# Kernel optimization log

Hardware: AMD Instinct MI355X
Metric: run time of the kernel (lower is better)

Reference implementation:

```python
import jax, jax.numpy as jnp
import numpy as np

B, S, HID, NH, INTER, VOCAB = 8, 1024, 512, 8, 2048, 30522
EPS = 1e-12


def _layernorm(x, w, b):
    m = jnp.mean(x, axis=-1, keepdims=True)
    v = jnp.mean((x - m) ** 2, axis=-1, keepdims=True)
    return (x - m) * jax.lax.rsqrt(v + EPS) * w + b


def _multihead_mut(x, M):
    # x: (b, s, d); M: (H, s, s). Split d into H heads, mix along the
    # sequence axis per head: out[b,t,h,d] = sum_s x[b,s,h,d] * M[h,s,t]
    b, s, d = x.shape
    xh = x.reshape(b, s, NH, d // NH)
    out = jnp.einsum('bshd,hst->bthd', xh, M)
    return out.reshape(b, s, d)


def setup_inputs() -> dict:
    key = jax.random.key(0)
    ks = jax.random.split(key, 14)
    g = lambda i, shape, scale: jax.random.normal(ks[i], shape, dtype=jnp.float32) * scale
    return {
        'x': jax.random.randint(ks[0], (B, S), 0, VOCAB),
        'word_emb': g(1, (VOCAB, HID), 0.02),
        'pos_emb': g(2, (S, HID), 0.02),
        'tok_emb': g(3, (2, HID), 0.02),
        'emb_ln_w': jnp.ones((HID,), dtype=jnp.float32),
        'emb_ln_b': jnp.zeros((HID,), dtype=jnp.float32),
        'init_d': g(4, (INTER, HID), 0.02),
        'init_b': g(5, (INTER,), 0.02),
        'init_M': g(6, (NH, S, S), 1.0 / np.sqrt(S)),
        'inter0_d': g(7, (INTER, INTER), 1.0 / np.sqrt(INTER)),
        'inter0_b': g(8, (INTER,), 0.02),
        'inter0_M': g(9, (NH, S, S), 1.0 / np.sqrt(S)),
        'final_d': g(10, (HID, INTER), 1.0 / np.sqrt(INTER)),
        'final_b': g(11, (HID,), 0.02),
    }


def reference(x, word_emb, pos_emb, tok_emb, emb_ln_w, emb_ln_b,
              init_d, init_b, init_M, inter0_d, inter0_b, inter0_M,
              final_d, final_b):
    # BertEmbeddings: word + position + token_type(all zeros) -> LayerNorm
    emb = word_emb[x] + pos_emb[None, :, :] + tok_emb[0][None, None, :]
    xo = _layernorm(emb, emb_ln_w, emb_ln_b)  # (B, S, HID)

    # layer 0 (flattened): project to intermediate, per-head seq mix, bias, quad act
    xo = xo @ init_d.T                      # (B, S, INTER)
    xo = _multihead_mut(xo, init_M)
    xo = xo + init_b
    xo = xo * xo                            # activation_quad

    # layer 1 (flattened)
    xo = xo @ inter0_d.T                    # (B, S, INTER)
    xo = _multihead_mut(xo, inter0_M)
    xo = xo + inter0_b
    xo = xo * xo                            # activation_quad

    return xo @ final_d.T + final_b         # (B, S, HID)
```

## Files before the change

kernel.cpp:

```cpp
#include <hip/hip_runtime.h>

typedef _Float16 f16;
typedef _Float16 f16x4 __attribute__((ext_vector_type(4)));
typedef _Float16 f16x8 __attribute__((ext_vector_type(8)));
typedef float    f32x4 __attribute__((ext_vector_type(4)));

#define SEQ   1024
#define HID   512
#define NHEAD 8
#define DH    256
#define INTER 2048
#define BATCH 8
#define ROWS  (BATCH * SEQ)

__device__ __forceinline__ void mm_core(const f16* __restrict__ At,
                                        const f16* __restrict__ Bt,
                                        int K, f32x4 (&acc)[4][4]) {
  __shared__ __align__(16) f16 As[128 * 32];
  __shared__ __align__(16) f16 Bs[128 * 32];
  const int tid  = threadIdx.x;
  const int lane = tid & 63, wv = tid >> 6;
  const int wm = (wv >> 1) * 64, wn = (wv & 1) * 64;
  const int lrow  = lane & 15;
  const int kfrag = (lane >> 4) * 8;
  const int c1 = wv * 64 + lane;
  const int r1 = c1 >> 2, kq1 = (c1 & 3) * 8;
  const int r2 = r1 + 64;
  const int eoff = c1 * 8;
  const f16* Ap1 = At + (size_t)r1 * K + kq1;
  const f16* Ap2 = At + (size_t)r2 * K + kq1;
  const f16* Bp1 = Bt + (size_t)r1 * K + kq1;
  const f16* Bp2 = Bt + (size_t)r2 * K + kq1;
  int4 ra1 = *(const int4*)Ap1;
  int4 ra2 = *(const int4*)Ap2;
  int4 rb1 = *(const int4*)Bp1;
  int4 rb2 = *(const int4*)Bp2;
  for (int k0 = 0; k0 < K; k0 += 32) {
    __syncthreads();
    *(int4*)&As[eoff]        = ra1;
    *(int4*)&As[2048 + eoff] = ra2;
    *(int4*)&Bs[eoff]        = rb1;
    *(int4*)&Bs[2048 + eoff] = rb2;
    __syncthreads();
    if (k0 + 32 < K) {
      ra1 = *(const int4*)(Ap1 + k0 + 32);
      ra2 = *(const int4*)(Ap2 + k0 + 32);
      rb1 = *(const int4*)(Bp1 + k0 + 32);
      rb2 = *(const int4*)(Bp2 + k0 + 32);
    }
    f16x8 af[4], bf[4];
    #pragma unroll
    for (int t = 0; t < 4; ++t) {
      af[t] = *(const f16x8*)&As[(wm + t * 16 + lrow) * 32 + kfrag];
      bf[t] = *(const f16x8*)&Bs[(wn + t * 16 + lrow) * 32 + kfrag];
    }
    #pragma unroll
    for (int i = 0; i < 4; ++i)
      #pragma unroll
      for (int j = 0; j < 4; ++j)
        acc[i][j] = __builtin_amdgcn_mfma_f32_16x16x32_f16(af[i], bf[j],
                                                           acc[i][j], 0, 0, 0);
  }
}

__device__ __forceinline__ void zero_acc(f32x4 (&acc)[4][4]) {
  f32x4 z = {0.f, 0.f, 0.f, 0.f};
  #pragma unroll
  for (int i = 0; i < 4; ++i)
    #pragma unroll
    for (int j = 0; j < 4; ++j) acc[i][j] = z;
}

__global__ __launch_bounds__(256) void gemm_t_kernel(
    const f16* __restrict__ A, const f16* __restrict__ W,
    f16* __restrict__ Xt, int K) {
  int row0 = blockIdx.y * 128, col0 = blockIdx.x * 128;
  f32x4 acc[4][4];
  zero_acc(acc);
  mm_core(A + (size_t)row0 * K, W + (size_t)col0 * K, K, acc);
  int tid = threadIdx.x, lane = tid & 63, wv = tid >> 6;
  int wm = (wv >> 1) * 64, wn = (wv & 1) * 64;
  int cn = lane & 15, rbase = (lane >> 4) * 4;
  int b = row0 >> 10, sbase = row0 & 1023;
  #pragma unroll
  for (int mt = 0; mt < 4; ++mt) {
    int s = sbase + wm + mt * 16 + rbase;
    #pragma unroll
    for (int nt = 0; nt < 4; ++nt) {
      int n = col0 + wn + nt * 16 + cn;
      int h = n >> 8, d = n & 255;
      f16x4 v = {(f16)acc[mt][nt][0], (f16)acc[mt][nt][1],
                 (f16)acc[mt][nt][2], (f16)acc[mt][nt][3]};
      *(f16x4*)&Xt[(((size_t)(b * 8 + h) * 256 + d) << 10) + s] = v;
    }
  }
}

__global__ __launch_bounds__(256) void mut_kernel(
    const f16* __restrict__ Mt, const f16* __restrict__ Xt,
    const float* __restrict__ bias, f16* __restrict__ Y) {
  int b = blockIdx.z >> 3, h = blockIdx.z & 7;
  int t0 = blockIdx.y * 128, d0 = blockIdx.x * 128;
  f32x4 acc[4][4];
  zero_acc(acc);
  const f16* Ap = Mt + ((size_t)h << 20) + ((size_t)t0 << 10);
  const f16* Bp = Xt + (((size_t)(b * 8 + h) * 256 + d0) << 10);
  mm_core(Ap, Bp, SEQ, acc);
  int tid = threadIdx.x, lane = tid & 63, wv = tid >> 6;
  int wm = (wv >> 1) * 64, wn = (wv & 1) * 64;
  int cn = lane & 15, rbase = (lane >> 4) * 4;
  #pragma unroll
  for (int mt = 0; mt < 4; ++mt) {
    int t = t0 + wm + mt * 16 + rbase;
    #pragma unroll
    for (int nt = 0; nt < 4; ++nt) {
      int d = d0 + wn + nt * 16 + cn;
      float bb = bias[(h << 8) + d];
      size_t base = (((size_t)(b << 10) + t) << 11) + (h << 8) + d;
      #pragma unroll
      for (int r = 0; r < 4; ++r) {
        float v = acc[mt][nt][r] + bb;
        Y[base + (size_t)r * INTER] = (f16)(v * v);
      }
    }
  }
}

__global__ __launch_bounds__(256) void gemm_out_kernel(
    const f16* __restrict__ A, const f16* __restrict__ W,
    const float* __restrict__ bias, float* __restrict__ out, int K, int N) {
  int row0 = blockIdx.y * 128, col0 = blockIdx.x * 128;
  f32x4 acc[4][4];
  zero_acc(acc);
  mm_core(A + (size_t)row0 * K, W + (size_t)col0 * K, K, acc);
  int tid = threadIdx.x, lane = tid & 63, wv = tid >> 6;
  int wm = (wv >> 1) * 64, wn = (wv & 1) * 64;
  int cn = lane & 15, rbase = (lane >> 4) * 4;
  #pragma unroll
  for (int mt = 0; mt < 4; ++mt) {
    int r0 = row0 + wm + mt * 16 + rbase;
    #pragma unroll
    for (int nt = 0; nt < 4; ++nt) {
      int col = col0 + wn + nt * 16 + cn;
      float bb = bias[col];
      #pragma unroll
      for (int r = 0; r < 4; ++r)
        out[(size_t)(r0 + r) * N + col] = acc[mt][nt][r] + bb;
    }
  }
}

__global__ __launch_bounds__(256) void embed_ln_kernel(
    const int* __restrict__ x, const float* __restrict__ wemb,
    const float* __restrict__ pemb, const float* __restrict__ temb,
    const float* __restrict__ lnw, const float* __restrict__ lnb,
    f16* __restrict__ out) {
  int row = blockIdx.x;
  int s = row & (SEQ - 1);
  int tok = x[row];
  const float* we = wemb + (size_t)tok * HID;
  const float* pe = pemb + (size_t)s * HID;
  int c = threadIdx.x;
  float e0 = we[c] + pe[c] + temb[c];
  float e1 = we[c + 256] + pe[c + 256] + temb[c + 256];
  float s1 = e0 + e1, s2 = e0 * e0 + e1 * e1;
  #pragma unroll
  for (int off = 32; off > 0; off >>= 1) {
    s1 += __shfl_down(s1, off, 64);
    s2 += __shfl_down(s2, off, 64);
  }
  __shared__ float r1[4], r2[4];
  int wid = threadIdx.x >> 6, lane = threadIdx.x & 63;
  if (lane == 0) { r1[wid] = s1; r2[wid] = s2; }
  __syncthreads();
  float S1 = r1[0] + r1[1] + r1[2] + r1[3];
  float S2 = r2[0] + r2[1] + r2[2] + r2[3];
  float m = S1 * (1.0f / HID);
  float v = S2 * (1.0f / HID) - m * m;
  float inv = rsqrtf(v + 1e-12f);
  f16* o = out + (size_t)row * HID;
  o[c]       = (f16)((e0 - m) * inv * lnw[c]       + lnb[c]);
  o[c + 256] = (f16)((e1 - m) * inv * lnw[c + 256] + lnb[c + 256]);
}

__global__ __launch_bounds__(256) void cast_f16_kernel(
    const float* __restrict__ in, f16* __restrict__ out, int n) {
  int i = (blockIdx.x * 256 + threadIdx.x) * 4;
  if (i < n) {
    float4 v = *(const float4*)(in + i);
    f16x4 o = {(f16)v.x, (f16)v.y, (f16)v.z, (f16)v.w};
    *(f16x4*)(out + i) = o;
  }
}

__global__ __launch_bounds__(256) void mtrans_kernel(
    const float* __restrict__ M, f16* __restrict__ Mt) {
  __shared__ float T[32][33];
  int h = blockIdx.z;
  int s0 = blockIdx.y * 32, t0 = blockIdx.x * 32;
  int tx = threadIdx.x & 31, ty = threadIdx.x >> 5;
  const float* Mh = M + ((size_t)h << 20);
  #pragma unroll
  for (int i = 0; i < 32; i += 8)
    T[ty + i][tx] = Mh[((size_t)(s0 + ty + i) << 10) + t0 + tx];
  __syncthreads();
  f16* Mth = Mt + ((size_t)h << 20);
  #pragma unroll
  for (int i = 0; i < 32; i += 8)
    Mth[((size_t)(t0 + ty + i) << 10) + s0 + tx] = (f16)T[tx][ty + i];
}

extern "C" void kernel_launch(void* const* d_in, const int* in_sizes, int n_in,
                              void* d_out, int out_size, void* d_ws, size_t ws_size,
                              hipStream_t stream) {
  const int*   x        = (const int*)d_in[0];
  const float* wemb     = (const float*)d_in[1];
  const float* pemb     = (const float*)d_in[2];
  const float* temb     = (const float*)d_in[3];
  const float* lnw      = (const float*)d_in[4];
  const float* lnb      = (const float*)d_in[5];
  const float* init_d   = (const float*)d_in[6];
  const float* init_b   = (const float*)d_in[7];
  const float* init_M   = (const float*)d_in[8];
  const float* inter0_d = (const float*)d_in[9];
  const float* inter0_b = (const float*)d_in[10];
  const float* inter0_M = (const float*)d_in[11];
  const float* final_d  = (const float*)d_in[12];
  const float* final_b  = (const float*)d_in[13];
  float* out = (float*)d_out;

  char* ws = (char*)d_ws;
  f16* R0 = (f16*)(ws);
  f16* R1 = (f16*)(ws + 8388608);
  f16* R2 = (f16*)(ws + 10485760);
  f16* R3 = (f16*)(ws + 27262976);
  f16* R4 = (f16*)(ws + 60817408);
  f16* R5 = (f16*)(ws + 94371840);

  embed_ln_kernel<<<ROWS, 256, 0, stream>>>(x, wemb, pemb, temb, lnw, lnb, R0);
  cast_f16_kernel<<<(INTER * HID / 4 + 255) / 256, 256, 0, stream>>>(init_d, R1, INTER * HID);
  mtrans_kernel<<<dim3(32, 32, 8), 256, 0, stream>>>(init_M, R2);
  gemm_t_kernel<<<dim3(INTER / 128, ROWS / 128), 256, 0, stream>>>(R0, R1, R3, HID);
  mut_kernel<<<dim3(DH / 128, SEQ / 128, BATCH * NHEAD), 256, 0, stream>>>(R2, R3, init_b, R4);
  cast_f16_kernel<<<(INTER * INTER / 4 + 255) / 256, 256, 0, stream>>>(inter0_d, R0, INTER * INTER);
  mtrans_kernel<<<dim3(32, 32, 8), 256, 0, stream>>>(inter0_M, R2);
  gemm_t_kernel<<<dim3(INTER / 128, ROWS / 128), 256, 0, stream>>>(R4, R0, R5, INTER);
  mut_kernel<<<dim3(DH / 128, SEQ / 128, BATCH * NHEAD), 256, 0, stream>>>(R2, R5, inter0_b, R3);
  cast_f16_kernel<<<(HID * INTER / 4 + 255) / 256, 256, 0, stream>>>(final_d, R1, HID * INTER);
  gemm_out_kernel<<<dim3(HID / 128, ROWS / 128), 256, 0, stream>>>(R3, R1, final_b, out, INTER, HID);
}
```

Before: 479.7 us.

## Double-buffer GEMM shared-memory tiles and XOR-swizzle LDS layout

The GEMM core now keeps two shared-memory stages. Each iteration writes the next K-slice into the alternate buffer while the MFMAs read the current one, which drops one of the two barriers per iteration. The LDS layout also applies an XOR swizzle on the k-offset by row to reduce bank conflicts on the fragment reads. In exchange, LDS use per block doubles, which may lower occupancy.

```diff
diff --git a/kernel.cpp b/kernel.cpp
--- a/kernel.cpp
+++ b/kernel.cpp
@@ -16,8 +16,8 @@
 __device__ __forceinline__ void mm_core(const f16* __restrict__ At,
                                         const f16* __restrict__ Bt,
                                         int K, f32x4 (&acc)[4][4]) {
-  __shared__ __align__(16) f16 As[128 * 32];
-  __shared__ __align__(16) f16 Bs[128 * 32];
+  __shared__ __align__(16) f16 As[2 * 4096];
+  __shared__ __align__(16) f16 Bs[2 * 4096];
   const int tid  = threadIdx.x;
   const int lane = tid & 63, wv = tid >> 6;
   const int wm = (wv >> 1) * 64, wn = (wv & 1) * 64;
@@ -26,7 +26,8 @@
   const int c1 = wv * 64 + lane;
   const int r1 = c1 >> 2, kq1 = (c1 & 3) * 8;
   const int r2 = r1 + 64;
-  const int eoff = c1 * 8;
+  const int e1 = r1 * 32 + (kq1 ^ (((r1 >> 1) & 3) << 3));
+  const int e2 = r2 * 32 + (kq1 ^ (((r2 >> 1) & 3) << 3));
   const f16* Ap1 = At + (size_t)r1 * K + kq1;
   const f16* Ap2 = At + (size_t)r2 * K + kq1;
   const f16* Bp1 = Bt + (size_t)r1 * K + kq1;
@@ -35,24 +36,46 @@
   int4 ra2 = *(const int4*)Ap2;
   int4 rb1 = *(const int4*)Bp1;
   int4 rb2 = *(const int4*)Bp2;
+  *(int4*)&As[e1] = ra1;
+  *(int4*)&As[e2] = ra2;
+  *(int4*)&Bs[e1] = rb1;
+  *(int4*)&Bs[e2] = rb2;
+  if (K > 32) {
+    ra1 = *(const int4*)(Ap1 + 32);
+    ra2 = *(const int4*)(Ap2 + 32);
+    rb1 = *(const int4*)(Bp1 + 32);
+    rb2 = *(const int4*)(Bp2 + 32);
+  }
+  int aoff[4], boff[4];
+  #pragma unroll
+  for (int t = 0; t < 4; ++t) {
+    int ra = wm + t * 16 + lrow;
+    aoff[t] = ra * 32 + (kfrag ^ (((ra >> 1) & 3) << 3));
+    int rb = wn + t * 16 + lrow;
+    boff[t] = rb * 32 + (kfrag ^ (((rb >> 1) & 3) << 3));
+  }
+  __syncthreads();
+  int cur = 0;
   for (int k0 = 0; k0 < K; k0 += 32) {
-    __syncthreads();
-    *(int4*)&As[eoff]        = ra1;
-    *(int4*)&As[2048 + eoff] = ra2;
-    *(int4*)&Bs[eoff]        = rb1;
-    *(int4*)&Bs[2048 + eoff] = rb2;
-    __syncthreads();
+    const int nxt = (cur ^ 1) * 4096;
     if (k0 + 32 < K) {
-      ra1 = *(const int4*)(Ap1 + k0 + 32);
-      ra2 = *(const int4*)(Ap2 + k0 + 32);
-      rb1 = *(const int4*)(Bp1 + k0 + 32);
-      rb2 = *(const int4*)(Bp2 + k0 + 32);
-    }
+      *(int4*)&As[nxt + e1] = ra1;
+      *(int4*)&As[nxt + e2] = ra2;
+      *(int4*)&Bs[nxt + e1] = rb1;
+      *(int4*)&Bs[nxt + e2] = rb2;
+      if (k0 + 64 < K) {
+        ra1 = *(const int4*)(Ap1 + k0 + 64);
+        ra2 = *(const int4*)(Ap2 + k0 + 64);
+        rb1 = *(const int4*)(Bp1 + k0 + 64);
+        rb2 = *(const int4*)(Bp2 + k0 + 64);
+      }
+    }
+    const int cb = cur * 4096;
     f16x8 af[4], bf[4];
     #pragma unroll
     for (int t = 0; t < 4; ++t) {
-      af[t] = *(const f16x8*)&As[(wm + t * 16 + lrow) * 32 + kfrag];
-      bf[t] = *(const f16x8*)&Bs[(wn + t * 16 + lrow) * 32 + kfrag];
+      af[t] = *(const f16x8*)&As[cb + aoff[t]];
+      bf[t] = *(const f16x8*)&Bs[cb + boff[t]];
     }
     #pragma unroll
     for (int i = 0; i < 4; ++i)
@@ -60,6 +83,8 @@
       for (int j = 0; j < 4; ++j)
         acc[i][j] = __builtin_amdgcn_mfma_f32_16x16x32_f16(af[i], bf[j],
                                                            acc[i][j], 0, 0, 0);
+    __syncthreads();
+    cur ^= 1;
   }
 }
 
```

Result: faster. 454.7 us (-5.2%).

## Replace LDS-staged GEMM core with direct global-to-register MFMA fragment loads

Applied to the files above, without the earlier changes.

Removes shared-memory staging and both block barriers from the shared GEMM core, so each wave loads its MFMA fragments straight from global memory into registers. The loads are double-buffered in registers across two 32-wide K steps. This drops LDS traffic and synchronisation. In exchange, each wave now fetches its own A and B tiles, so the wave pair sharing a tile row or column loads it twice and L2/global traffic doubles. The 16-byte per-lane loads also stride across rows, which hurts coalescing.

```diff
diff --git a/kernel.cpp b/kernel.cpp
--- a/kernel.cpp
+++ b/kernel.cpp
@@ -13,52 +13,50 @@
 #define BATCH 8
 #define ROWS  (BATCH * SEQ)
 
-__device__ __forceinline__ void mm_core(const f16* __restrict__ At,
-                                        const f16* __restrict__ Bt,
-                                        int K, f32x4 (&acc)[4][4]) {
-  __shared__ __align__(16) f16 As[128 * 32];
-  __shared__ __align__(16) f16 Bs[128 * 32];
-  const int tid  = threadIdx.x;
-  const int lane = tid & 63, wv = tid >> 6;
+__device__ __forceinline__ void mm_direct(const f16* __restrict__ At,
+                                          const f16* __restrict__ Bt,
+                                          int K, f32x4 (&acc)[4][4]) {
+  const int lane = threadIdx.x & 63, wv = threadIdx.x >> 6;
   const int wm = (wv >> 1) * 64, wn = (wv & 1) * 64;
   const int lrow  = lane & 15;
   const int kfrag = (lane >> 4) * 8;
-  const int c1 = wv * 64 + lane;
-  const int r1 = c1 >> 2, kq1 = (c1 & 3) * 8;
-  const int r2 = r1 + 64;
-  const int eoff = c1 * 8;
-  const f16* Ap1 = At + (size_t)r1 * K + kq1;
-  const f16* Ap2 = At + (size_t)r2 * K + kq1;
-  const f16* Bp1 = Bt + (size_t)r1 * K + kq1;
-  const f16* Bp2 = Bt + (size_t)r2 * K + kq1;
-  int4 ra1 = *(const int4*)Ap1;
-  int4 ra2 = *(const int4*)Ap2;
-  int4 rb1 = *(const int4*)Bp1;
-  int4 rb2 = *(const int4*)Bp2;
-  for (int k0 = 0; k0 < K; k0 += 32) {
-    __syncthreads();
-    *(int4*)&As[eoff]        = ra1;
-    *(int4*)&As[2048 + eoff] = ra2;
-    *(int4*)&Bs[eoff]        = rb1;
-    *(int4*)&Bs[2048 + eoff] = rb2;
-    __syncthreads();
-    if (k0 + 32 < K) {
-      ra1 = *(const int4*)(Ap1 + k0 + 32);
-      ra2 = *(const int4*)(Ap2 + k0 + 32);
-      rb1 = *(const int4*)(Bp1 + k0 + 32);
-      rb2 = *(const int4*)(Bp2 + k0 + 32);
-    }
-    f16x8 af[4], bf[4];
+  const f16* ap[4];
+  const f16* bp[4];
+  #pragma unroll
+  for (int t = 0; t < 4; ++t) {
+    ap[t] = At + (size_t)(wm + t * 16 + lrow) * K + kfrag;
+    bp[t] = Bt + (size_t)(wn + t * 16 + lrow) * K + kfrag;
+  }
+  f16x8 a0[4], b0[4], a1[4], b1[4];
+  #pragma unroll
+  for (int t = 0; t < 4; ++t) {
+    a0[t] = *(const f16x8*)(ap[t]);
+    b0[t] = *(const f16x8*)(bp[t]);
+  }
+  for (int k0 = 0; k0 < K; k0 += 64) {
     #pragma unroll
     for (int t = 0; t < 4; ++t) {
-      af[t] = *(const f16x8*)&As[(wm + t * 16 + lrow) * 32 + kfrag];
-      bf[t] = *(const f16x8*)&Bs[(wn + t * 16 + lrow) * 32 + kfrag];
+      a1[t] = *(const f16x8*)(ap[t] + k0 + 32);
+      b1[t] = *(const f16x8*)(bp[t] + k0 + 32);
     }
     #pragma unroll
     for (int i = 0; i < 4; ++i)
       #pragma unroll
       for (int j = 0; j < 4; ++j)
-        acc[i][j] = __builtin_amdgcn_mfma_f32_16x16x32_f16(af[i], bf[j],
+        acc[i][j] = __builtin_amdgcn_mfma_f32_16x16x32_f16(a0[i], b0[j],
+                                                           acc[i][j], 0, 0, 0);
+    if (k0 + 64 < K) {
+      #pragma unroll
+      for (int t = 0; t < 4; ++t) {
+        a0[t] = *(const f16x8*)(ap[t] + k0 + 64);
+        b0[t] = *(const f16x8*)(bp[t] + k0 + 64);
+      }
+    }
+    #pragma unroll
+    for (int i = 0; i < 4; ++i)
+      #pragma unroll
+      for (int j = 0; j < 4; ++j)
+        acc[i][j] = __builtin_amdgcn_mfma_f32_16x16x32_f16(a1[i], b1[j],
                                                            acc[i][j], 0, 0, 0);
   }
 }
@@ -77,7 +75,7 @@
   int row0 = blockIdx.y * 128, col0 = blockIdx.x * 128;
   f32x4 acc[4][4];
   zero_acc(acc);
-  mm_core(A + (size_t)row0 * K, W + (size_t)col0 * K, K, acc);
+  mm_direct(A + (size_t)row0 * K, W + (size_t)col0 * K, K, acc);
   int tid = threadIdx.x, lane = tid & 63, wv = tid >> 6;
   int wm = (wv >> 1) * 64, wn = (wv & 1) * 64;
   int cn = lane & 15, rbase = (lane >> 4) * 4;
@@ -105,7 +103,7 @@
   zero_acc(acc);
   const f16* Ap = Mt + ((size_t)h << 20) + ((size_t)t0 << 10);
   const f16* Bp = Xt + (((size_t)(b * 8 + h) * 256 + d0) << 10);
-  mm_core(Ap, Bp, SEQ, acc);
+  mm_direct(Ap, Bp, SEQ, acc);
   int tid = threadIdx.x, lane = tid & 63, wv = tid >> 6;
   int wm = (wv >> 1) * 64, wn = (wv & 1) * 64;
   int cn = lane & 15, rbase = (lane >> 4) * 4;
@@ -132,7 +130,7 @@
   int row0 = blockIdx.y * 128, col0 = blockIdx.x * 128;
   f32x4 acc[4][4];
   zero_acc(acc);
-  mm_core(A + (size_t)row0 * K, W + (size_t)col0 * K, K, acc);
+  mm_direct(A + (size_t)row0 * K, W + (size_t)col0 * K, K, acc);
   int tid = threadIdx.x, lane = tid & 63, wv = tid >> 6;
   int wm = (wv >> 1) * 64, wn = (wv & 1) * 64;
   int cn = lane & 15, rbase = (lane >> 4) * 4;
```

Measured after the change: 814.7 us. 69.8% more time.

## Load GEMM tiles directly into LDS with swizzle and merge matrix transposes

Applied to the files above, without the earlier changes.

Replaces register-staged global loads in the shared GEMM core with global_load_lds direct-to-LDS transfers and an XOR-swizzled tile layout so that fragment reads avoid bank conflicts. The register prefetch of the next tile is removed, so loads and MFMA compute in each K step are now serialized behind a full wait and barrier. The two sequence-mixing matrix transposes are also fused into one launch, which needs a separate workspace buffer for the second transposed matrix.

```diff
diff --git a/kernel.cpp b/kernel.cpp
--- a/kernel.cpp
+++ b/kernel.cpp
@@ -13,46 +13,54 @@
 #define BATCH 8
 #define ROWS  (BATCH * SEQ)
 
+__device__ __forceinline__ void load16_lds(const void* g, void* l) {
+  __builtin_amdgcn_global_load_lds(
+      (const __attribute__((address_space(1))) unsigned int*)g,
+      (__attribute__((address_space(3))) unsigned int*)l, 16, 0, 0);
+}
+
 __device__ __forceinline__ void mm_core(const f16* __restrict__ At,
                                         const f16* __restrict__ Bt,
-                                        int K, f32x4 (&acc)[4][4]) {
-  __shared__ __align__(16) f16 As[128 * 32];
-  __shared__ __align__(16) f16 Bs[128 * 32];
+                                        int K, int ld, f32x4 (&acc)[4][4]) {
+  __shared__ __align__(16) f16 As[4096];
+  __shared__ __align__(16) f16 Bs[4096];
   const int tid  = threadIdx.x;
   const int lane = tid & 63, wv = tid >> 6;
   const int wm = (wv >> 1) * 64, wn = (wv & 1) * 64;
   const int lrow  = lane & 15;
-  const int kfrag = (lane >> 4) * 8;
+  const int qf    = lane >> 4;
   const int c1 = wv * 64 + lane;
-  const int r1 = c1 >> 2, kq1 = (c1 & 3) * 8;
-  const int r2 = r1 + 64;
-  const int eoff = c1 * 8;
-  const f16* Ap1 = At + (size_t)r1 * K + kq1;
-  const f16* Ap2 = At + (size_t)r2 * K + kq1;
-  const f16* Bp1 = Bt + (size_t)r1 * K + kq1;
-  const f16* Bp2 = Bt + (size_t)r2 * K + kq1;
-  int4 ra1 = *(const int4*)Ap1;
-  int4 ra2 = *(const int4*)Ap2;
-  int4 rb1 = *(const int4*)Bp1;
-  int4 rb2 = *(const int4*)Bp2;
+  const int r1 = c1 >> 2, q1 = (c1 & 3) ^ ((r1 >> 1) & 3);
+  const int c2 = c1 + 256;
+  const int r2 = c2 >> 2, q2 = (c2 & 3) ^ ((r2 >> 1) & 3);
+  const f16* Ap1 = At + (size_t)r1 * ld + q1 * 8;
+  const f16* Ap2 = At + (size_t)r2 * ld + q2 * 8;
+  const f16* Bp1 = Bt + (size_t)r1 * ld + q1 * 8;
+  const f16* Bp2 = Bt + (size_t)r2 * ld + q2 * 8;
+  f16* As1 = &As[wv * 512];
+  f16* As2 = &As[2048 + wv * 512];
+  f16* Bs1 = &Bs[wv * 512];
+  f16* Bs2 = &Bs[2048 + wv * 512];
+  int aoff[4], boff[4];
+  #pragma unroll
+  for (int t = 0; t < 4; ++t) {
+    int ra = wm + t * 16 + lrow;
+    aoff[t] = ra * 32 + ((qf ^ ((ra >> 1) & 3)) << 3);
+    int rb = wn + t * 16 + lrow;
+    boff[t] = rb * 32 + ((qf ^ ((rb >> 1) & 3)) << 3);
+  }
   for (int k0 = 0; k0 < K; k0 += 32) {
+    load16_lds(Ap1 + k0, As1);
+    load16_lds(Ap2 + k0, As2);
+    load16_lds(Bp1 + k0, Bs1);
+    load16_lds(Bp2 + k0, Bs2);
+    __builtin_amdgcn_s_waitcnt(0x0F70);
     __syncthreads();
-    *(int4*)&As[eoff]        = ra1;
-    *(int4*)&As[2048 + eoff] = ra2;
-    *(int4*)&Bs[eoff]        = rb1;
-    *(int4*)&Bs[2048 + eoff] = rb2;
-    __syncthreads();
-    if (k0 + 32 < K) {
-      ra1 = *(const int4*)(Ap1 + k0 + 32);
-      ra2 = *(const int4*)(Ap2 + k0 + 32);
-      rb1 = *(const int4*)(Bp1 + k0 + 32);
-      rb2 = *(const int4*)(Bp2 + k0 + 32);
-    }
     f16x8 af[4], bf[4];
     #pragma unroll
     for (int t = 0; t < 4; ++t) {
-      af[t] = *(const f16x8*)&As[(wm + t * 16 + lrow) * 32 + kfrag];
-      bf[t] = *(const f16x8*)&Bs[(wn + t * 16 + lrow) * 32 + kfrag];
+      af[t] = *(const f16x8*)&As[aoff[t]];
+      bf[t] = *(const f16x8*)&Bs[boff[t]];
     }
     #pragma unroll
     for (int i = 0; i < 4; ++i)
@@ -60,6 +68,7 @@
       for (int j = 0; j < 4; ++j)
         acc[i][j] = __builtin_amdgcn_mfma_f32_16x16x32_f16(af[i], bf[j],
                                                            acc[i][j], 0, 0, 0);
+    __syncthreads();
   }
 }
 
@@ -77,7 +86,7 @@
   int row0 = blockIdx.y * 128, col0 = blockIdx.x * 128;
   f32x4 acc[4][4];
   zero_acc(acc);
-  mm_core(A + (size_t)row0 * K, W + (size_t)col0 * K, K, acc);
+  mm_core(A + (size_t)row0 * K, W + (size_t)col0 * K, K, K, acc);
   int tid = threadIdx.x, lane = tid & 63, wv = tid >> 6;
   int wm = (wv >> 1) * 64, wn = (wv & 1) * 64;
   int cn = lane & 15, rbase = (lane >> 4) * 4;
@@ -105,7 +114,7 @@
   zero_acc(acc);
   const f16* Ap = Mt + ((size_t)h << 20) + ((size_t)t0 << 10);
   const f16* Bp = Xt + (((size_t)(b * 8 + h) * 256 + d0) << 10);
-  mm_core(Ap, Bp, SEQ, acc);
+  mm_core(Ap, Bp, SEQ, SEQ, acc);
   int tid = threadIdx.x, lane = tid & 63, wv = tid >> 6;
   int wm = (wv >> 1) * 64, wn = (wv & 1) * 64;
   int cn = lane & 15, rbase = (lane >> 4) * 4;
@@ -132,7 +141,7 @@
   int row0 = blockIdx.y * 128, col0 = blockIdx.x * 128;
   f32x4 acc[4][4];
   zero_acc(acc);
-  mm_core(A + (size_t)row0 * K, W + (size_t)col0 * K, K, acc);
+  mm_core(A + (size_t)row0 * K, W + (size_t)col0 * K, K, K, acc);
   int tid = threadIdx.x, lane = tid & 63, wv = tid >> 6;
   int wm = (wv >> 1) * 64, wn = (wv & 1) * 64;
   int cn = lane & 15, rbase = (lane >> 4) * 4;
@@ -193,18 +202,20 @@
   }
 }
 
-__global__ __launch_bounds__(256) void mtrans_kernel(
-    const float* __restrict__ M, f16* __restrict__ Mt) {
+__global__ __launch_bounds__(256) void mtrans2_kernel(
+    const float* __restrict__ M1, const float* __restrict__ M2,
+    f16* __restrict__ Mt1, f16* __restrict__ Mt2) {
   __shared__ float T[32][33];
-  int h = blockIdx.z;
+  int z = blockIdx.z;
+  int h = z & 7;
+  const float* Mh = (z < 8 ? M1 : M2) + ((size_t)h << 20);
+  f16* Mth = (z < 8 ? Mt1 : Mt2) + ((size_t)h << 20);
   int s0 = blockIdx.y * 32, t0 = blockIdx.x * 32;
   int tx = threadIdx.x & 31, ty = threadIdx.x >> 5;
-  const float* Mh = M + ((size_t)h << 20);
   #pragma unroll
   for (int i = 0; i < 32; i += 8)
     T[ty + i][tx] = Mh[((size_t)(s0 + ty + i) << 10) + t0 + tx];
   __syncthreads();
-  f16* Mth = Mt + ((size_t)h << 20);
   #pragma unroll
   for (int i = 0; i < 32; i += 8)
     Mth[((size_t)(t0 + ty + i) << 10) + s0 + tx] = (f16)T[tx][ty + i];
@@ -230,22 +241,22 @@
   float* out = (float*)d_out;
 
   char* ws = (char*)d_ws;
-  f16* R0 = (f16*)(ws);
-  f16* R1 = (f16*)(ws + 8388608);
-  f16* R2 = (f16*)(ws + 10485760);
-  f16* R3 = (f16*)(ws + 27262976);
-  f16* R4 = (f16*)(ws + 60817408);
-  f16* R5 = (f16*)(ws + 94371840);
+  f16*   R0  = (f16*)(ws);
+  f16*   R1  = (f16*)(ws + 8388608);
+  f16*   Mt1 = (f16*)(ws + 10485760);
+  f16*   Mt2 = (f16*)(ws + 27262976);
+  f16*   R3  = (f16*)(ws + 44040192);
+  f16*   R4  = (f16*)(ws + 77594624);
+  f16*   R5  = (f16*)(ws + 111149056);
 
   embed_ln_kernel<<<ROWS, 256, 0, stream>>>(x, wemb, pemb, temb, lnw, lnb, R0);
   cast_f16_kernel<<<(INTER * HID / 4 + 255) / 256, 256, 0, stream>>>(init_d, R1, INTER * HID);
-  mtrans_kernel<<<dim3(32, 32, 8), 256, 0, stream>>>(init_M, R2);
+  mtrans2_kernel<<<dim3(32, 32, 16), 256, 0, stream>>>(init_M, inter0_M, Mt1, Mt2);
   gemm_t_kernel<<<dim3(INTER / 128, ROWS / 128), 256, 0, stream>>>(R0, R1, R3, HID);
-  mut_kernel<<<dim3(DH / 128, SEQ / 128, BATCH * NHEAD), 256, 0, stream>>>(R2, R3, init_b, R4);
+  mut_kernel<<<dim3(DH / 128, SEQ / 128, BATCH * NHEAD), 256, 0, stream>>>(Mt1, R3, init_b, R4);
   cast_f16_kernel<<<(INTER * INTER / 4 + 255) / 256, 256, 0, stream>>>(inter0_d, R0, INTER * INTER);
-  mtrans_kernel<<<dim3(32, 32, 8), 256, 0, stream>>>(inter0_M, R2);
   gemm_t_kernel<<<dim3(INTER / 128, ROWS / 128), 256, 0, stream>>>(R4, R0, R5, INTER);
-  mut_kernel<<<dim3(DH / 128, SEQ / 128, BATCH * NHEAD), 256, 0, stream>>>(R2, R5, inter0_b, R3);
+  mut_kernel<<<dim3(DH / 128, SEQ / 128, BATCH * NHEAD), 256, 0, stream>>>(Mt2, R5, inter0_b, R3);
   cast_f16_kernel<<<(HID * INTER / 4 + 255) / 256, 256, 0, stream>>>(final_d, R1, HID * INTER);
   gemm_out_kernel<<<dim3(HID / 128, ROWS / 128), 256, 0, stream>>>(R3, R1, final_b, out, INTER, HID);
 }
```

Result: slower. 492.3 us (+2.6%).
